# Optimization experiments

Measured on AMD Instinct MI355X. Metric: run time of the kernel, lower is better.

The kernel has to match this reference:

```python
import jax, jax.numpy as jnp
import numpy as np

P = 16          # patch size
IMG = 224       # image size
EPS_COMBINE = 2.220446049250313e-16  # np.finfo(float).eps
NOISE_EPS = 0.01
LOSS_COEF = 1e-2
K = 1


def _patchify(x):
    # x: [B, C, H, W] -> [B, n_patches, C*P*P] (channel-major flatten, matching conv weight layout)
    B, C, H, W = x.shape
    gh, gw = H // P, W // P
    x = x.reshape(B, C, gh, P, gw, P)
    x = x.transpose(0, 2, 4, 1, 3, 5).reshape(B, gh * gw, C * P * P)
    return x


def _cv_squared(v):
    # squared coefficient of variation; torch .var() is unbiased (ddof=1)
    return jnp.var(v, ddof=1) / (jnp.mean(v) ** 2 + 1e-10)


def _norm_cdf(v):
    return jax.scipy.stats.norm.cdf(v)


def setup_inputs() -> dict:
    key = jax.random.key(0)
    ks = jax.random.split(key, 7)
    B, E, D_IN = 64, 8, 320
    x = jax.random.normal(ks[0], (B, 3, IMG, IMG), dtype=jnp.float32)
    g = jax.random.normal(ks[1], (B, D_IN), dtype=jnp.float32)
    noise = jax.random.normal(ks[2], (B, E), dtype=jnp.float32)
    w_gate = jax.random.normal(ks[3], (D_IN, E), dtype=jnp.float32) * 0.02
    w_noise = jax.random.normal(ks[4], (D_IN, E), dtype=jnp.float32) * 0.02
    w_exp = jax.random.normal(ks[5], (E, 768, 3, P, P), dtype=jnp.float32) * 0.02
    b_exp = jnp.zeros((E, 768), dtype=jnp.float32)
    return {"x": x, "g": g, "noise": noise, "w_gate": w_gate,
            "w_noise": w_noise, "w_exp": w_exp, "b_exp": b_exp}


def reference(x, g, noise, w_gate, w_noise, w_exp, b_exp):
    B = x.shape[0]
    E = w_gate.shape[1]

    # ---- noisy top-k gating (train mode) ----
    clean_logits = g @ w_gate                                   # [B, E]
    noise_stddev = jax.nn.softplus(g @ w_noise) + NOISE_EPS     # [B, E]
    noisy_logits = clean_logits + noise * noise_stddev          # [B, E]

    top_logits, top_idx = jax.lax.top_k(noisy_logits, K + 1)    # [B, K+1]
    top_k_gates = jax.nn.softmax(top_logits[:, :K], axis=1)     # [B, K]
    gates = jnp.zeros_like(noisy_logits).at[
        jnp.arange(B)[:, None], top_idx[:, :K]].set(top_k_gates)  # [B, E]

    # load: prob each expert's noisy logit lands in top-k (differentiable balance term)
    thr_in = top_logits[:, K][:, None]       # (k+1)-th value per row
    thr_out = top_logits[:, K - 1][:, None]  # k-th value per row
    is_in = noisy_logits > thr_in
    prob = jnp.where(is_in,
                     _norm_cdf((clean_logits - thr_in) / noise_stddev),
                     _norm_cdf((clean_logits - thr_out) / noise_stddev))
    load = prob.sum(0)                                           # [E]
    importance = gates.sum(0)                                    # [E]
    loss = (_cv_squared(importance) + _cv_squared(load)) * LOSS_COEF

    # ---- experts: per-expert patch-embed conv == patchify + GEMM ----
    patches = _patchify(x)                                       # [B, 196, 768]
    wf = w_exp.reshape(E, w_exp.shape[1], -1)                    # [E, out=768, in=768]
    y_exp = jnp.einsum('bpi,eoi->ebpo', patches, wf) + b_exp[:, None, None, :]  # [E,B,196,768]

    # ---- gate-weighted combine (dense equivalent of dispatch/combine) ----
    y = jnp.einsum('be,ebpo->bpo', gates, y_exp)                 # [B, 196, 768]
    y = jnp.where(y == 0, jnp.asarray(EPS_COMBINE, y.dtype), y)  # combined[combined==0] = eps
    return y, loss
```

## Files before the change

### kernel.cpp

```cpp
#include <hip/hip_runtime.h>
#include <math.h>

typedef unsigned short u16;
typedef unsigned int   u32;

using bf16x8 = __attribute__((ext_vector_type(8))) short;
using f32x4  = __attribute__((ext_vector_type(4))) float;

#define NB   64
#define NE   8
#define DIN  320
#define NP   196
#define MPAD 256
#define CK   768
#define CN   768

#define BM 128
#define BN 128
#define BK 32
#define NKT (CK / BK)

__device__ __forceinline__ u16 f2bf(float f) {
    u32 u = __builtin_bit_cast(u32, f);
    u += 0x7fffu + ((u >> 16) & 1u);
    return (u16)(u >> 16);
}

__device__ __forceinline__ void gload16(const void* g, void* l) {
    __builtin_amdgcn_global_load_lds(
        (const __attribute__((address_space(1))) void*)g,
        (__attribute__((address_space(3))) void*)l, 16, 0, 0);
}

__global__ __launch_bounds__(256) void gate1_kernel(
    const float* __restrict__ g,
    const float* __restrict__ noise,
    const float* __restrict__ w_gate,
    const float* __restrict__ w_noise,
    float* __restrict__ gCl, float* __restrict__ gSd, float* __restrict__ gNy)
{
    __shared__ float sW[DIN][NE];
    __shared__ float sWn[DIN][NE];
    __shared__ float sG[8][DIN];
    const int t  = threadIdx.x;
    const int b0 = blockIdx.x * 8;
    for (int i = t; i < DIN * NE; i += 256) {
        sW[i >> 3][i & 7]  = w_gate[i];
        sWn[i >> 3][i & 7] = w_noise[i];
        sG[i / DIN][i % DIN] = g[b0 * DIN + i];
    }
    __syncthreads();
    const int pair = t >> 2, q = t & 3;
    const int bl = pair >> 3, e = pair & 7;
    float cl = 0.f, nz = 0.f;
    const int i0 = q * 80;
    #pragma unroll 4
    for (int j = 0; j < 80; ++j) {
        float gv = sG[bl][i0 + j];
        cl = fmaf(gv, sW[i0 + j][e], cl);
        nz = fmaf(gv, sWn[i0 + j][e], nz);
    }
    cl += __shfl_xor(cl, 1); cl += __shfl_xor(cl, 2);
    nz += __shfl_xor(nz, 1); nz += __shfl_xor(nz, 2);
    if (q == 0) {
        int p = (b0 + bl) * NE + e;
        float sd = fmaxf(nz, 0.f) + log1pf(expf(-fabsf(nz))) + 0.01f;
        gCl[p] = cl; gSd[p] = sd;
        gNy[p] = fmaf(noise[p], sd, cl);
    }
}

__global__ __launch_bounds__(512) void gate2_kernel(
    const float* __restrict__ gCl,
    const float* __restrict__ gSd,
    const float* __restrict__ gNy,
    int* __restrict__ eid,
    float* __restrict__ loss_out)
{
    __shared__ float sNy[NB][NE];
    __shared__ float sProb[NB][NE];
    __shared__ int   sTop[NB];
    __shared__ float sImp[NE], sLoad[NE];
    const int t = threadIdx.x;
    const int b = t >> 3, e = t & 7;
    float cl = gCl[t], sd = gSd[t], ny = gNy[t];
    sNy[b][e] = ny;
    __syncthreads();
    float v1 = -1e30f, v2 = -1e30f; int i1 = 0;
    #pragma unroll
    for (int k2 = 0; k2 < NE; ++k2) {
        float v = sNy[b][k2];
        if (v > v1) { v2 = v1; v1 = v; i1 = k2; }
        else if (v > v2) { v2 = v; }
    }
    if (e == 0) { sTop[b] = i1; eid[b] = i1; }
    float thr = (ny > v2) ? v2 : v1;
    float z = (cl - thr) / sd;
    sProb[b][e] = 0.5f * (1.0f + erff(z * 0.7071067811865476f));
    __syncthreads();
    if (t < NE) {
        float imp = 0.f, ld = 0.f;
        for (int i = 0; i < NB; ++i) {
            imp += (sTop[i] == t) ? 1.0f : 0.0f;
            ld  += sProb[i][t];
        }
        sImp[t] = imp; sLoad[t] = ld;
    }
    __syncthreads();
    if (t == 0) {
        float mi = 0.f, ml = 0.f;
        for (int k2 = 0; k2 < NE; ++k2) { mi += sImp[k2]; ml += sLoad[k2]; }
        mi *= (1.0f / NE); ml *= (1.0f / NE);
        float vi = 0.f, vl = 0.f;
        for (int k2 = 0; k2 < NE; ++k2) {
            float d1 = sImp[k2] - mi;  vi += d1 * d1;
            float d2 = sLoad[k2] - ml; vl += d2 * d2;
        }
        vi *= (1.0f / (NE - 1)); vl *= (1.0f / (NE - 1));
        loss_out[0] = (vi / (mi * mi + 1e-10f) + vl / (ml * ml + 1e-10f)) * 0.01f;
    }
}

__global__ void wconv_kernel(const float* __restrict__ w, u16* __restrict__ wb)
{
    int idx = blockIdx.x * 256 + threadIdx.x;
    const float* src = w + (size_t)idx * 8;
    float4 f0 = *reinterpret_cast<const float4*>(src);
    float4 f1 = *reinterpret_cast<const float4*>(src + 4);
    uint4 o;
    o.x = (u32)f2bf(f0.x) | ((u32)f2bf(f0.y) << 16);
    o.y = (u32)f2bf(f0.z) | ((u32)f2bf(f0.w) << 16);
    o.z = (u32)f2bf(f1.x) | ((u32)f2bf(f1.y) << 16);
    o.w = (u32)f2bf(f1.z) | ((u32)f2bf(f1.w) << 16);
    *reinterpret_cast<uint4*>(wb + (size_t)idx * 8) = o;
}

__global__ void patchify_kernel(const float* __restrict__ x, u16* __restrict__ patches)
{
    int idx = blockIdx.x * 256 + threadIdx.x;
    int i8   = idx % 96;
    int rest = idx / 96;
    int p    = rest % NP;
    int b    = rest / NP;
    u16* dst = patches + ((size_t)(b * MPAD + p)) * CK + i8 * 8;
    int gh = p / 14, gw = p % 14;
    int i0  = i8 * 8;
    int c   = i0 >> 8;
    int rem = i0 & 255;
    int ph  = rem >> 4;
    int pw0 = rem & 15;
    const float* src = x + (((size_t)(b * 3 + c) * 224 + gh * 16 + ph) * 224 + gw * 16 + pw0);
    float4 f0 = *reinterpret_cast<const float4*>(src);
    float4 f1 = *reinterpret_cast<const float4*>(src + 4);
    uint4 o;
    o.x = (u32)f2bf(f0.x) | ((u32)f2bf(f0.y) << 16);
    o.y = (u32)f2bf(f0.z) | ((u32)f2bf(f0.w) << 16);
    o.z = (u32)f2bf(f1.x) | ((u32)f2bf(f1.y) << 16);
    o.w = (u32)f2bf(f1.z) | ((u32)f2bf(f1.w) << 16);
    *reinterpret_cast<uint4*>(dst) = o;
}

__global__ __launch_bounds__(256) void gemm_kernel(
    const u16* __restrict__ patches,
    const u16* __restrict__ wb,
    const float* __restrict__ b_exp,
    const int* __restrict__ eid,
    float* __restrict__ out)
{
    __shared__ char smem[2][16384];

    const int id = blockIdx.x;
    const int v  = (id & 7) * 96 + (id >> 3);
    const int b  = v / 12;
    const int rr = v % 12;
    const int m0 = (rr / 6) * BM;
    const int n0 = (rr % 6) * BN;
    const int e  = eid[b];

    const int t  = threadIdx.x;
    const int l  = t & 63;
    const int w  = t >> 6;
    const int wm = w >> 1;
    const int wn = w & 1;

    const int rs = (w << 5) + (l >> 2);
    const u32 cg = (u32)((l & 3) ^ (l >> 4));
    const u16* aSrc = patches + ((size_t)(b * MPAD) + m0 + rs) * CK + cg * 8;
    const u16* bSrc = wb + (size_t)e * CK * CN + (size_t)(n0 + rs) * CK + cg * 8;
    const u32 lOff = (u32)(w * 2048);
    char* smem0 = &smem[0][0];

    u32 aOff[4], bOff[4];
    #pragma unroll
    for (int fm = 0; fm < 4; ++fm) {
        int row = wm * 64 + fm * 16 + (l & 15);
        u32 c = (u32)(l >> 4) ^ (u32)((row >> 2) & 3);
        aOff[fm] = (u32)row * 64 + c * 16;
    }
    #pragma unroll
    for (int fn = 0; fn < 4; ++fn) {
        int row = wn * 64 + fn * 16 + (l & 15);
        u32 c = (u32)(l >> 4) ^ (u32)((row >> 2) & 3);
        bOff[fn] = (u32)row * 64 + c * 16;
    }

    f32x4 acc[4][4];
    #pragma unroll
    for (int fm = 0; fm < 4; ++fm)
        #pragma unroll
        for (int fn = 0; fn < 4; ++fn)
            acc[fm][fn] = (f32x4){0.f, 0.f, 0.f, 0.f};

    gload16(aSrc,           smem0 + lOff);
    gload16(aSrc + 16 * CK, smem0 + lOff + 1024);
    gload16(bSrc,           smem0 + 8192 + lOff);
    gload16(bSrc + 16 * CK, smem0 + 8192 + lOff + 1024);
    aSrc += BK; bSrc += BK;

    for (int kt = 0; kt < NKT - 1; ++kt) {
        char* sn = smem0 + (u32)(((kt + 1) & 1) * 16384);
        gload16(aSrc,           sn + lOff);
        gload16(aSrc + 16 * CK, sn + lOff + 1024);
        gload16(bSrc,           sn + 8192 + lOff);
        gload16(bSrc + 16 * CK, sn + 8192 + lOff + 1024);
        aSrc += BK; bSrc += BK;

        asm volatile("s_waitcnt vmcnt(4)" ::: "memory");
        __builtin_amdgcn_s_barrier();

        char* sc = smem0 + (u32)((kt & 1) * 16384);
        bf16x8 af[4], bfr[4];
        #pragma unroll
        for (int fm = 0; fm < 4; ++fm)
            af[fm] = *reinterpret_cast<const bf16x8*>(sc + aOff[fm]);
        #pragma unroll
        for (int fn = 0; fn < 4; ++fn)
            bfr[fn] = *reinterpret_cast<const bf16x8*>(sc + 8192 + bOff[fn]);

        #pragma unroll
        for (int fm = 0; fm < 4; ++fm)
            #pragma unroll
            for (int fn = 0; fn < 4; ++fn)
                acc[fm][fn] = __builtin_amdgcn_mfma_f32_16x16x32_bf16(
                    af[fm], bfr[fn], acc[fm][fn], 0, 0, 0);

        __builtin_amdgcn_s_barrier();
    }

    asm volatile("s_waitcnt vmcnt(0)" ::: "memory");
    __builtin_amdgcn_s_barrier();
    {
        char* sc = smem0 + (u32)(((NKT - 1) & 1) * 16384);
        bf16x8 af[4], bfr[4];
        #pragma unroll
        for (int fm = 0; fm < 4; ++fm)
            af[fm] = *reinterpret_cast<const bf16x8*>(sc + aOff[fm]);
        #pragma unroll
        for (int fn = 0; fn < 4; ++fn)
            bfr[fn] = *reinterpret_cast<const bf16x8*>(sc + 8192 + bOff[fn]);
        #pragma unroll
        for (int fm = 0; fm < 4; ++fm)
            #pragma unroll
            for (int fn = 0; fn < 4; ++fn)
                acc[fm][fn] = __builtin_amdgcn_mfma_f32_16x16x32_bf16(
                    af[fm], bfr[fn], acc[fm][fn], 0, 0, 0);
    }

    const int r4 = (l >> 4) * 4;
    #pragma unroll
    for (int fm = 0; fm < 4; ++fm) {
        int mb = m0 + wm * 64 + fm * 16 + r4;
        #pragma unroll
        for (int fn = 0; fn < 4; ++fn) {
            int col = n0 + wn * 64 + fn * 16 + (l & 15);
            float bias = b_exp[e * CN + col];
            #pragma unroll
            for (int q = 0; q < 4; ++q) {
                int mrow = mb + q;
                if (mrow < NP) {
                    float vv = acc[fm][fn][q] + bias;
                    if (vv == 0.0f) vv = 2.220446049250313e-16f;
                    out[((size_t)b * NP + mrow) * CN + col] = vv;
                }
            }
        }
    }
}

extern "C" void kernel_launch(void* const* d_in, const int* in_sizes, int n_in,
                              void* d_out, int out_size, void* d_ws, size_t ws_size,
                              hipStream_t stream) {
    const float* x       = (const float*)d_in[0];
    const float* g       = (const float*)d_in[1];
    const float* noise   = (const float*)d_in[2];
    const float* w_gate  = (const float*)d_in[3];
    const float* w_noise = (const float*)d_in[4];
    const float* w_exp   = (const float*)d_in[5];
    const float* b_exp   = (const float*)d_in[6];
    float* out = (float*)d_out;

    char* ws = (char*)d_ws;
    int*   eid     = (int*)ws;
    float* gCl     = (float*)(ws + 256);
    float* gSd     = (float*)(ws + 256 + 2048);
    float* gNy     = (float*)(ws + 256 + 4096);
    u16*   patches = (u16*)(ws + 8192);
    u16*   wbf     = (u16*)(ws + 8192 + (size_t)NB * MPAD * CK * 2);

    hipLaunchKernelGGL(gate1_kernel, dim3(8), dim3(256), 0, stream,
                       g, noise, w_gate, w_noise, gCl, gSd, gNy);
    hipLaunchKernelGGL(gate2_kernel, dim3(1), dim3(512), 0, stream,
                       gCl, gSd, gNy, eid, out + (size_t)NB * NP * CN);
    hipLaunchKernelGGL(wconv_kernel, dim3((NE * CN * CK / 8) / 256), dim3(256), 0, stream,
                       w_exp, wbf);
    hipLaunchKernelGGL(patchify_kernel, dim3((NB * NP * 96) / 256), dim3(256), 0, stream,
                       x, patches);
    hipLaunchKernelGGL(gemm_kernel, dim3(CN / BN * MPAD / BM * NB), dim3(256), 0, stream,
                       patches, wbf, b_exp, eid, out);
}
```

Before: 69.17 us.

## Fuse patchify into GEMM A-load and merge gating with weight conversion

The GEMM now reads fp32 image pixels straight from x, converts them to bf16 in registers and writes them into swizzled LDS, software-pipelined one k-step ahead. This removes the separate patchify kernel and its padded bf16 patch buffer round-trip through global memory. The gate-logit computation and the expert-weight bf16 conversion are merged into one launch, dropping a kernel launch. The GEMM moves to 512 threads with 8 waves each covering 32x64 tiles, and A conversion uses a cheaper round-half-up packing that can differ slightly from round-to-nearest-even.

```diff
diff --git a/kernel.cpp b/kernel.cpp
--- a/kernel.cpp
+++ b/kernel.cpp
@@ -11,7 +11,6 @@
 #define NE   8
 #define DIN  320
 #define NP   196
-#define MPAD 256
 #define CK   768
 #define CN   768
 
@@ -20,54 +19,78 @@
 #define BK 32
 #define NKT (CK / BK)
 
+#define WCONV_BLOCKS 2304
+
 __device__ __forceinline__ u16 f2bf(float f) {
     u32 u = __builtin_bit_cast(u32, f);
     u += 0x7fffu + ((u >> 16) & 1u);
     return (u16)(u >> 16);
 }
 
+__device__ __forceinline__ u32 pkbf(float a, float b) {
+    u32 ua = (__builtin_bit_cast(u32, a) + 0x8000u) >> 16;
+    u32 ub = (__builtin_bit_cast(u32, b) + 0x8000u) & 0xffff0000u;
+    return ua | ub;
+}
+
 __device__ __forceinline__ void gload16(const void* g, void* l) {
     __builtin_amdgcn_global_load_lds(
         (const __attribute__((address_space(1))) void*)g,
         (__attribute__((address_space(3))) void*)l, 16, 0, 0);
 }
 
-__global__ __launch_bounds__(256) void gate1_kernel(
+__global__ __launch_bounds__(256) void prep1_kernel(
     const float* __restrict__ g,
     const float* __restrict__ noise,
     const float* __restrict__ w_gate,
     const float* __restrict__ w_noise,
-    float* __restrict__ gCl, float* __restrict__ gSd, float* __restrict__ gNy)
+    const float* __restrict__ w_exp,
+    float* __restrict__ gCl, float* __restrict__ gSd, float* __restrict__ gNy,
+    u16* __restrict__ wb)
 {
-    __shared__ float sW[DIN][NE];
-    __shared__ float sWn[DIN][NE];
-    __shared__ float sG[8][DIN];
-    const int t  = threadIdx.x;
-    const int b0 = blockIdx.x * 8;
-    for (int i = t; i < DIN * NE; i += 256) {
-        sW[i >> 3][i & 7]  = w_gate[i];
-        sWn[i >> 3][i & 7] = w_noise[i];
-        sG[i / DIN][i % DIN] = g[b0 * DIN + i];
-    }
-    __syncthreads();
-    const int pair = t >> 2, q = t & 3;
-    const int bl = pair >> 3, e = pair & 7;
-    float cl = 0.f, nz = 0.f;
-    const int i0 = q * 80;
-    #pragma unroll 4
-    for (int j = 0; j < 80; ++j) {
-        float gv = sG[bl][i0 + j];
-        cl = fmaf(gv, sW[i0 + j][e], cl);
-        nz = fmaf(gv, sWn[i0 + j][e], nz);
-    }
-    cl += __shfl_xor(cl, 1); cl += __shfl_xor(cl, 2);
-    nz += __shfl_xor(nz, 1); nz += __shfl_xor(nz, 2);
-    if (q == 0) {
-        int p = (b0 + bl) * NE + e;
-        float sd = fmaxf(nz, 0.f) + log1pf(expf(-fabsf(nz))) + 0.01f;
-        gCl[p] = cl; gSd[p] = sd;
-        gNy[p] = fmaf(noise[p], sd, cl);
-    }
+    __shared__ float sW[DIN][NE + 1];
+    __shared__ float sWn[DIN][NE + 1];
+    const int t = threadIdx.x;
+    int bid = blockIdx.x;
+
+    if (bid < 8) {
+        for (int i = t; i < DIN * NE; i += 256) {
+            sW[i >> 3][i & 7]  = w_gate[i];
+            sWn[i >> 3][i & 7] = w_noise[i];
+        }
+        __syncthreads();
+        const int pair = t >> 2, q = t & 3;
+        const int bl = pair >> 3, e = pair & 7;
+        const int b = bid * 8 + bl;
+        float cl = 0.f, nz = 0.f;
+        const float* gr = g + b * DIN + q * 80;
+        #pragma unroll 4
+        for (int j = 0; j < 80; ++j) {
+            float gv = gr[j];
+            cl = fmaf(gv, sW[q * 80 + j][e], cl);
+            nz = fmaf(gv, sWn[q * 80 + j][e], nz);
+        }
+        cl += __shfl_xor(cl, 1); cl += __shfl_xor(cl, 2);
+        nz += __shfl_xor(nz, 1); nz += __shfl_xor(nz, 2);
+        if (q == 0) {
+            int p = b * NE + e;
+            float sd = fmaxf(nz, 0.f) + log1pf(expf(-fabsf(nz))) + 0.01f;
+            gCl[p] = cl; gSd[p] = sd;
+            gNy[p] = fmaf(noise[p], sd, cl);
+        }
+        return;
+    }
+    bid -= 8;
+    int idx = bid * 256 + t;
+    const float* src = w_exp + (size_t)idx * 8;
+    float4 f0 = *reinterpret_cast<const float4*>(src);
+    float4 f1 = *reinterpret_cast<const float4*>(src + 4);
+    uint4 o;
+    o.x = (u32)f2bf(f0.x) | ((u32)f2bf(f0.y) << 16);
+    o.y = (u32)f2bf(f0.z) | ((u32)f2bf(f0.w) << 16);
+    o.z = (u32)f2bf(f1.x) | ((u32)f2bf(f1.y) << 16);
+    o.w = (u32)f2bf(f1.z) | ((u32)f2bf(f1.w) << 16);
+    *reinterpret_cast<uint4*>(wb + (size_t)idx * 8) = o;
 }
 
 __global__ __launch_bounds__(512) void gate2_kernel(
@@ -121,47 +144,8 @@
     }
 }
 
-__global__ void wconv_kernel(const float* __restrict__ w, u16* __restrict__ wb)
-{
-    int idx = blockIdx.x * 256 + threadIdx.x;
-    const float* src = w + (size_t)idx * 8;
-    float4 f0 = *reinterpret_cast<const float4*>(src);
-    float4 f1 = *reinterpret_cast<const float4*>(src + 4);
-    uint4 o;
-    o.x = (u32)f2bf(f0.x) | ((u32)f2bf(f0.y) << 16);
-    o.y = (u32)f2bf(f0.z) | ((u32)f2bf(f0.w) << 16);
-    o.z = (u32)f2bf(f1.x) | ((u32)f2bf(f1.y) << 16);
-    o.w = (u32)f2bf(f1.z) | ((u32)f2bf(f1.w) << 16);
-    *reinterpret_cast<uint4*>(wb + (size_t)idx * 8) = o;
-}
-
-__global__ void patchify_kernel(const float* __restrict__ x, u16* __restrict__ patches)
-{
-    int idx = blockIdx.x * 256 + threadIdx.x;
-    int i8   = idx % 96;
-    int rest = idx / 96;
-    int p    = rest % NP;
-    int b    = rest / NP;
-    u16* dst = patches + ((size_t)(b * MPAD + p)) * CK + i8 * 8;
-    int gh = p / 14, gw = p % 14;
-    int i0  = i8 * 8;
-    int c   = i0 >> 8;
-    int rem = i0 & 255;
-    int ph  = rem >> 4;
-    int pw0 = rem & 15;
-    const float* src = x + (((size_t)(b * 3 + c) * 224 + gh * 16 + ph) * 224 + gw * 16 + pw0);
-    float4 f0 = *reinterpret_cast<const float4*>(src);
-    float4 f1 = *reinterpret_cast<const float4*>(src + 4);
-    uint4 o;
-    o.x = (u32)f2bf(f0.x) | ((u32)f2bf(f0.y) << 16);
-    o.y = (u32)f2bf(f0.z) | ((u32)f2bf(f0.w) << 16);
-    o.z = (u32)f2bf(f1.x) | ((u32)f2bf(f1.y) << 16);
-    o.w = (u32)f2bf(f1.z) | ((u32)f2bf(f1.w) << 16);
-    *reinterpret_cast<uint4*>(dst) = o;
-}
-
-__global__ __launch_bounds__(256) void gemm_kernel(
-    const u16* __restrict__ patches,
+__global__ __launch_bounds__(512) void gemm_kernel(
+    const float* __restrict__ x,
     const u16* __restrict__ wb,
     const float* __restrict__ b_exp,
     const int* __restrict__ eid,
@@ -183,93 +167,94 @@
     const int wm = w >> 1;
     const int wn = w & 1;
 
-    const int rs = (w << 5) + (l >> 2);
     const u32 cg = (u32)((l & 3) ^ (l >> 4));
-    const u16* aSrc = patches + ((size_t)(b * MPAD) + m0 + rs) * CK + cg * 8;
-    const u16* bSrc = wb + (size_t)e * CK * CN + (size_t)(n0 + rs) * CK + cg * 8;
-    const u32 lOff = (u32)(w * 2048);
-    char* smem0 = &smem[0][0];
-
-    u32 aOff[4], bOff[4];
-    #pragma unroll
-    for (int fm = 0; fm < 4; ++fm) {
-        int row = wm * 64 + fm * 16 + (l & 15);
-        u32 c = (u32)(l >> 4) ^ (u32)((row >> 2) & 3);
-        aOff[fm] = (u32)row * 64 + c * 16;
+    const u16* bS = wb + (size_t)e * (CK * CN)
+                  + (size_t)(n0 + (w << 4) + (l >> 2)) * CK + cg * 8;
+    const u32 bLds = 8192u + ((u32)w << 10) + ((u32)l << 4);
+
+    const int arow = t >> 2;
+    int p = m0 + arow; if (p > NP - 1) p = NP - 1;
+    const int gh = p / 14, gw = p % 14;
+    const int seg = (t & 3) >> 1, pw0 = (t & 1) * 8;
+    const float* xb = x + (size_t)b * 150528 + (gh * 16 + seg) * 224 + gw * 16 + pw0;
+    const u32 wA = (u32)(arow * 64 + (((t & 3) ^ ((arow >> 2) & 3)) << 4));
+
+    u32 aOff[2], bOff[4];
+    #pragma unroll
+    for (int fm = 0; fm < 2; ++fm) {
+        int row = wm * 32 + fm * 16 + (l & 15);
+        aOff[fm] = (u32)(row * 64) + (((u32)(l >> 4) ^ (u32)((row >> 2) & 3)) << 4);
     }
     #pragma unroll
     for (int fn = 0; fn < 4; ++fn) {
         int row = wn * 64 + fn * 16 + (l & 15);
-        u32 c = (u32)(l >> 4) ^ (u32)((row >> 2) & 3);
-        bOff[fn] = (u32)row * 64 + c * 16;
-    }
-
-    f32x4 acc[4][4];
-    #pragma unroll
-    for (int fm = 0; fm < 4; ++fm)
+        bOff[fn] = 8192u + (u32)(row * 64) + (((u32)(l >> 4) ^ (u32)((row >> 2) & 3)) << 4);
+    }
+
+    f32x4 acc[2][4];
+    #pragma unroll
+    for (int fm = 0; fm < 2; ++fm)
         #pragma unroll
         for (int fn = 0; fn < 4; ++fn)
             acc[fm][fn] = (f32x4){0.f, 0.f, 0.f, 0.f};
 
-    gload16(aSrc,           smem0 + lOff);
-    gload16(aSrc + 16 * CK, smem0 + lOff + 1024);
-    gload16(bSrc,           smem0 + 8192 + lOff);
-    gload16(bSrc + 16 * CK, smem0 + 8192 + lOff + 1024);
-    aSrc += BK; bSrc += BK;
-
-    for (int kt = 0; kt < NKT - 1; ++kt) {
-        char* sn = smem0 + (u32)(((kt + 1) & 1) * 16384);
-        gload16(aSrc,           sn + lOff);
-        gload16(aSrc + 16 * CK, sn + lOff + 1024);
-        gload16(bSrc,           sn + 8192 + lOff);
-        gload16(bSrc + 16 * CK, sn + 8192 + lOff + 1024);
-        aSrc += BK; bSrc += BK;
-
-        asm volatile("s_waitcnt vmcnt(4)" ::: "memory");
+    char* smem0 = &smem[0][0];
+
+    {
+        float4 ra0 = *reinterpret_cast<const float4*>(xb);
+        float4 ra1 = *reinterpret_cast<const float4*>(xb + 4);
+        __builtin_amdgcn_sched_barrier(0);
+        gload16(bS, smem0 + bLds);
+        __builtin_amdgcn_sched_barrier(0);
+        uint4 o;
+        o.x = pkbf(ra0.x, ra0.y); o.y = pkbf(ra0.z, ra0.w);
+        o.z = pkbf(ra1.x, ra1.y); o.w = pkbf(ra1.z, ra1.w);
+        *reinterpret_cast<uint4*>(smem0 + wA) = o;
+        asm volatile("s_waitcnt lgkmcnt(0)" ::: "memory");
         __builtin_amdgcn_s_barrier();
-
-        char* sc = smem0 + (u32)((kt & 1) * 16384);
-        bf16x8 af[4], bfr[4];
-        #pragma unroll
-        for (int fm = 0; fm < 4; ++fm)
-            af[fm] = *reinterpret_cast<const bf16x8*>(sc + aOff[fm]);
+    }
+
+    for (int kt = 0; kt < NKT; ++kt) {
+        const int kn = (kt + 1 < NKT) ? kt + 1 : NKT - 1;
+        const int koff = (kn >> 3) * 50176 + (kn & 7) * 448;
+        char* bufn = smem0 + (u32)(((kt + 1) & 1) * 16384);
+        char* bufc = smem0 + (u32)((kt & 1) * 16384);
+
+        float4 ra0 = *reinterpret_cast<const float4*>(xb + koff);
+        float4 ra1 = *reinterpret_cast<const float4*>(xb + koff + 4);
+        __builtin_amdgcn_sched_barrier(0);
+        gload16(bS + kn * BK, bufn + bLds);
+        __builtin_amdgcn_sched_barrier(0);
+        asm volatile("s_waitcnt vmcnt(3)" ::: "memory");
+        __builtin_amdgcn_s_barrier();
+
+        bf16x8 af[2], bfr[4];
+        #pragma unroll
+        for (int fm = 0; fm < 2; ++fm)
+            af[fm] = *reinterpret_cast<const bf16x8*>(bufc + aOff[fm]);
         #pragma unroll
         for (int fn = 0; fn < 4; ++fn)
-            bfr[fn] = *reinterpret_cast<const bf16x8*>(sc + 8192 + bOff[fn]);
-
-        #pragma unroll
-        for (int fm = 0; fm < 4; ++fm)
+            bfr[fn] = *reinterpret_cast<const bf16x8*>(bufc + bOff[fn]);
+
+        #pragma unroll
+        for (int fm = 0; fm < 2; ++fm)
             #pragma unroll
             for (int fn = 0; fn < 4; ++fn)
                 acc[fm][fn] = __builtin_amdgcn_mfma_f32_16x16x32_bf16(
                     af[fm], bfr[fn], acc[fm][fn], 0, 0, 0);
 
+        uint4 o;
+        o.x = pkbf(ra0.x, ra0.y); o.y = pkbf(ra0.z, ra0.w);
+        o.z = pkbf(ra1.x, ra1.y); o.w = pkbf(ra1.z, ra1.w);
+        *reinterpret_cast<uint4*>(bufn + wA) = o;
+        asm volatile("s_waitcnt lgkmcnt(0)" ::: "memory");
         __builtin_amdgcn_s_barrier();
     }
 
-    asm volatile("s_waitcnt vmcnt(0)" ::: "memory");
-    __builtin_amdgcn_s_barrier();
-    {
-        char* sc = smem0 + (u32)(((NKT - 1) & 1) * 16384);
-        bf16x8 af[4], bfr[4];
-        #pragma unroll
-        for (int fm = 0; fm < 4; ++fm)
-            af[fm] = *reinterpret_cast<const bf16x8*>(sc + aOff[fm]);
-        #pragma unroll
-        for (int fn = 0; fn < 4; ++fn)
-            bfr[fn] = *reinterpret_cast<const bf16x8*>(sc + 8192 + bOff[fn]);
-        #pragma unroll
-        for (int fm = 0; fm < 4; ++fm)
-            #pragma unroll
-            for (int fn = 0; fn < 4; ++fn)
-                acc[fm][fn] = __builtin_amdgcn_mfma_f32_16x16x32_bf16(
-                    af[fm], bfr[fn], acc[fm][fn], 0, 0, 0);
-    }
-
     const int r4 = (l >> 4) * 4;
     #pragma unroll
-    for (int fm = 0; fm < 4; ++fm) {
-        int mb = m0 + wm * 64 + fm * 16 + r4;
+    for (int fm = 0; fm < 2; ++fm) {
+        int mb = m0 + wm * 32 + fm * 16 + r4;
         #pragma unroll
         for (int fn = 0; fn < 4; ++fn) {
             int col = n0 + wn * 64 + fn * 16 + (l & 15);
@@ -300,21 +285,16 @@
     float* out = (float*)d_out;
 
     char* ws = (char*)d_ws;
-    int*   eid     = (int*)ws;
-    float* gCl     = (float*)(ws + 256);
-    float* gSd     = (float*)(ws + 256 + 2048);
-    float* gNy     = (float*)(ws + 256 + 4096);
-    u16*   patches = (u16*)(ws + 8192);
-    u16*   wbf     = (u16*)(ws + 8192 + (size_t)NB * MPAD * CK * 2);
-
-    hipLaunchKernelGGL(gate1_kernel, dim3(8), dim3(256), 0, stream,
-                       g, noise, w_gate, w_noise, gCl, gSd, gNy);
+    int*   eid = (int*)ws;
+    float* gCl = (float*)(ws + 256);
+    float* gSd = (float*)(ws + 2304);
+    float* gNy = (float*)(ws + 4352);
+    u16*   wbf = (u16*)(ws + 8192);
+
+    hipLaunchKernelGGL(prep1_kernel, dim3(8 + WCONV_BLOCKS), dim3(256), 0, stream,
+                       g, noise, w_gate, w_noise, w_exp, gCl, gSd, gNy, wbf);
     hipLaunchKernelGGL(gate2_kernel, dim3(1), dim3(512), 0, stream,
                        gCl, gSd, gNy, eid, out + (size_t)NB * NP * CN);
-    hipLaunchKernelGGL(wconv_kernel, dim3((NE * CN * CK / 8) / 256), dim3(256), 0, stream,
-                       w_exp, wbf);
-    hipLaunchKernelGGL(patchify_kernel, dim3((NB * NP * 96) / 256), dim3(256), 0, stream,
-                       x, patches);
-    hipLaunchKernelGGL(gemm_kernel, dim3(CN / BN * MPAD / BM * NB), dim3(256), 0, stream,
-                       patches, wbf, b_exp, eid, out);
-}
+    hipLaunchKernelGGL(gemm_kernel, dim3(CN / BN * (2 * NB)), dim3(512), 0, stream,
+                       x, wbf, b_exp, eid, out);
+}
```

New measurement: 58.01 us. -16.1%, faster.
